# Kernel optimization log

Hardware: AMD Instinct MI355X
Metric: run time of the kernel (lower is better)

The kernel has to match this reference:

```python
import jax, jax.numpy as jnp
import numpy as np

B, S, DIM = 1, 2048, 2048
NH, NKV, HD = 32, 8, 64
NREP = NH // NKV  # 4


def setup_inputs() -> dict:
    key = jax.random.key(0)
    ks = jax.random.split(key, 5)
    x = jax.random.normal(ks[0], (B, S, DIM), jnp.float32)
    # torch nn.Linear weight layout: (out_features, in_features)
    wq = jax.random.normal(ks[1], (NH * HD, DIM), jnp.float32) * (DIM ** -0.5)
    wk = jax.random.normal(ks[2], (NKV * HD, DIM), jnp.float32) * (DIM ** -0.5)
    wv = jax.random.normal(ks[3], (NKV * HD, DIM), jnp.float32) * (DIM ** -0.5)
    wo = jax.random.normal(ks[4], (DIM, NH * HD), jnp.float32) * ((NH * HD) ** -0.5)
    # Llama-style rotary frequencies: angle[t, i] = t / 10000^(2i/head_dim)
    inv_freq = 1.0 / (10000.0 ** (np.arange(0, HD, 2, dtype=np.float64) / HD))  # (HD/2,)
    ang = np.outer(np.arange(S, dtype=np.float64), inv_freq)                     # (S, HD/2)
    freqs_cis = jnp.asarray(np.stack([np.cos(ang), np.sin(ang)], axis=-1), jnp.float32)  # (S, HD/2, 2)
    # additive causal mask, shape (1, 1, S, S)
    mask = jnp.triu(jnp.full((S, S), -1e9, jnp.float32), k=1)[None, None]
    return dict(x=x, wq=wq, wk=wk, wv=wv, wo=wo, freqs_cis=freqs_cis, mask=mask)


def _apply_rope(x, cos, sin):
    # x: (B, S, H, HD); rotate adjacent pairs along last dim
    xr = x.reshape(x.shape[:-1] + (-1, 2))
    x1, x2 = xr[..., 0], xr[..., 1]
    c = cos[None, :, None, :]  # (1, S, 1, HD/2)
    s = sin[None, :, None, :]
    out = jnp.stack([x1 * c - x2 * s, x1 * s + x2 * c], axis=-1)
    return out.reshape(x.shape)


def reference(x, wq, wk, wv, wo, freqs_cis, mask):
    b, s, _ = x.shape
    q = (x @ wq.T).reshape(b, s, NH, HD)
    k = (x @ wk.T).reshape(b, s, NKV, HD)
    v = (x @ wv.T).reshape(b, s, NKV, HD)
    cos, sin = freqs_cis[..., 0], freqs_cis[..., 1]
    q = _apply_rope(q, cos, sin)
    k = _apply_rope(k, cos, sin)
    # GQA: group q heads by kv head instead of materializing repeated K/V
    qg = q.reshape(b, s, NKV, NREP, HD)
    scale = HD ** -0.5
    # scores: (b, g=kv_head, r=rep, s=q_pos, t=k_pos)
    scores = jnp.einsum('bsgrd,btgd->bgrst', qg, k) * scale
    scores = scores + mask[:, :, None]  # (1,1,1,S,S) broadcast
    p = jax.nn.softmax(scores.astype(jnp.float32), axis=-1).astype(q.dtype)
    out = jnp.einsum('bgrst,btgd->bsgrd', p, v).reshape(b, s, NH * HD)
    return out @ wo.T
```

## Files before the change

kernel.cpp:

```cpp
#include <hip/hip_runtime.h>
#include <hip/hip_bf16.h>

#define S_LEN 2048
#define DIM_  2048
#define NH    32
#define NKV   8
#define HD    64

typedef __bf16 bf16x8 __attribute__((ext_vector_type(8)));
typedef __bf16 bf16x4 __attribute__((ext_vector_type(4)));
typedef float  f32x4  __attribute__((ext_vector_type(4)));

#define AS_GLOBAL(p) ((const __attribute__((address_space(1))) void*)(p))
#define AS_LDS(p)    ((__attribute__((address_space(3))) void*)(p))

__global__ __launch_bounds__(256) void cvt_xw(
    const float* __restrict__ x,  const float* __restrict__ wq,
    const float* __restrict__ wk, const float* __restrict__ wv,
    const float* __restrict__ wo,
    __bf16* __restrict__ xb, __bf16* __restrict__ wb, __bf16* __restrict__ wob)
{
  const size_t stride = 458752;
  size_t base = (size_t)blockIdx.x * 256 + threadIdx.x;
#pragma unroll
  for (int k = 0; k < 8; ++k) {
    size_t i = base + (size_t)k * stride;
    const float* src; __bf16* dst; size_t off;
    if (i < 1048576)      { src = x;  dst = xb;            off = i; }
    else if (i < 2097152) { src = wq; dst = wb;            off = i - 1048576; }
    else if (i < 2359296) { src = wk; dst = wb + 4194304;  off = i - 2097152; }
    else if (i < 2621440) { src = wv; dst = wb + 5242880;  off = i - 2359296; }
    else                  { src = wo; dst = wob;           off = i - 2621440; }
    float4 f = ((const float4*)src)[off];
    bf16x4 r;
    r[0] = (__bf16)f.x; r[1] = (__bf16)f.y; r[2] = (__bf16)f.z; r[3] = (__bf16)f.w;
    ((bf16x4*)dst)[off] = r;
  }
}

#define BK 32
#define TA_ELEMS 4096
#define TB_ELEMS 2048

__device__ __forceinline__ void stage_A(
    const __bf16* __restrict__ g, int row0, int k0, int ld, __bf16* lds)
{
  const int tid = threadIdx.x;
  const int wave = tid >> 6;
#pragma unroll
  for (int iss = 0; iss < 2; ++iss) {
    int off = (iss * 256 + tid) * 16;
    int r = off >> 6;
    int c = (off & 63) >> 1;
    __builtin_amdgcn_global_load_lds(
        AS_GLOBAL(g + (size_t)(row0 + r) * ld + k0 + c),
        AS_LDS(lds + iss * 2048 + wave * 512),
        16, 0, 0);
  }
}

__device__ __forceinline__ void stage_B(
    const __bf16* __restrict__ g, int row0, int k0, int ld, __bf16* lds)
{
  const int tid = threadIdx.x;
  int off = tid * 16;
  int r = off >> 6;
  int c = (off & 63) >> 1;
  __builtin_amdgcn_global_load_lds(
      AS_GLOBAL(g + (size_t)(row0 + r) * ld + k0 + c),
      AS_LDS(lds + (tid >> 6) * 512), 16, 0, 0);
}

__device__ __forceinline__ void gemm_mainloop(
    const __bf16* __restrict__ A, const __bf16* __restrict__ B,
    int row0, int col0, int lda, int ldb, int nt,
    __bf16* As, __bf16* Bs, f32x4 acc[4][2])
{
  const int lane = threadIdx.x & 63;
  const int wave = threadIdx.x >> 6;
  const int wr = wave >> 1, wc = wave & 1;
  const int fr = lane & 15, fg = lane >> 4;

  stage_A(A, row0, 0, lda, As);
  stage_B(B, col0, 0, ldb, Bs);

  for (int t = 0; t < nt; ++t) {
    const int cur = t & 1;
    if (t + 1 < nt) {
      stage_A(A, row0, (t + 1) * BK, lda, As + (cur ^ 1) * TA_ELEMS);
      stage_B(B, col0, (t + 1) * BK, ldb, Bs + (cur ^ 1) * TB_ELEMS);
    }
    __syncthreads();
    bf16x8 a[4], b[2];
#pragma unroll
    for (int mi = 0; mi < 4; ++mi)
      a[mi] = *(const bf16x8*)(As + cur * TA_ELEMS + (wr * 64 + mi * 16 + fr) * 32 + fg * 8);
#pragma unroll
    for (int ni = 0; ni < 2; ++ni)
      b[ni] = *(const bf16x8*)(Bs + cur * TB_ELEMS + (wc * 32 + ni * 16 + fr) * 32 + fg * 8);
#pragma unroll
    for (int mi = 0; mi < 4; ++mi)
#pragma unroll
      for (int ni = 0; ni < 2; ++ni)
        acc[mi][ni] = __builtin_amdgcn_mfma_f32_16x16x32_bf16(a[mi], b[ni], acc[mi][ni], 0, 0, 0);
    __syncthreads();
  }
}

__global__ __launch_bounds__(256) void qkv_gemm(
    const __bf16* __restrict__ xb, const __bf16* __restrict__ wb,
    __bf16* __restrict__ q_buf, __bf16* __restrict__ k_buf, __bf16* __restrict__ v_buf)
{
  __shared__ __bf16 As[2 * TA_ELEMS];
  __shared__ __bf16 Bs[2 * TB_ELEMS];
  const int lane = threadIdx.x & 63;
  const int wave = threadIdx.x >> 6;
  const int wr = wave >> 1, wc = wave & 1;
  const int fr = lane & 15, fg = lane >> 4;

  const int lid = blockIdx.x;
  const int xcd = lid & 7;
  const int i   = lid >> 3;
  const int row0 = (i & 15) * 128;
  const int col0 = (xcd * 6 + (i >> 4)) * 64;

  f32x4 acc[4][2] = {};
  gemm_mainloop(xb, wb, row0, col0, DIM_, DIM_, DIM_ / BK, As, Bs, acc);

  const int rowg0 = row0 + wr * 64;
  const int colg0 = col0 + wc * 32;
#pragma unroll
  for (int mi = 0; mi < 4; ++mi) {
#pragma unroll
    for (int ni = 0; ni < 2; ++ni) {
#pragma unroll
      for (int j = 0; j < 4; ++j) {
        int row = rowg0 + mi * 16 + fg * 4 + j;
        int col = colg0 + ni * 16 + fr;
        float v = acc[mi][ni][j];
        if (col < 2048) {
          int h = col >> 6, d = col & 63;
          q_buf[((size_t)h * S_LEN + row) * HD + d] = (__bf16)v;
        } else if (col < 2560) {
          int c = col - 2048, g = c >> 6, d = c & 63;
          k_buf[((size_t)g * S_LEN + row) * HD + d] = (__bf16)v;
        } else {
          int c = col - 2560, g = c >> 6, d = c & 63;
          v_buf[((size_t)g * HD + d) * S_LEN + row] = (__bf16)v;
        }
      }
    }
  }
}

__global__ __launch_bounds__(256) void oproj_gemm(
    const __bf16* __restrict__ attn_buf, const __bf16* __restrict__ wob,
    float* __restrict__ out)
{
  __shared__ __bf16 As[2 * TA_ELEMS];
  __shared__ __bf16 Bs[2 * TB_ELEMS];
  const int lane = threadIdx.x & 63;
  const int wave = threadIdx.x >> 6;
  const int wr = wave >> 1, wc = wave & 1;
  const int fr = lane & 15, fg = lane >> 4;

  const int lid = blockIdx.x;
  const int xcd = lid & 7;
  const int i   = lid >> 3;
  const int row0 = (i & 15) * 128;
  const int col0 = (xcd * 4 + (i >> 4)) * 64;

  f32x4 acc[4][2] = {};
  gemm_mainloop(attn_buf, wob, row0, col0, DIM_, DIM_, DIM_ / BK, As, Bs, acc);

  const int rowg0 = row0 + wr * 64;
  const int colg0 = col0 + wc * 32;
#pragma unroll
  for (int mi = 0; mi < 4; ++mi)
#pragma unroll
    for (int ni = 0; ni < 2; ++ni)
#pragma unroll
      for (int j = 0; j < 4; ++j) {
        int row = rowg0 + mi * 16 + fg * 4 + j;
        int col = colg0 + ni * 16 + fr;
        out[(size_t)row * DIM_ + col] = acc[mi][ni][j];
      }
}

__global__ __launch_bounds__(256) void rope_k(
    __bf16* __restrict__ k_buf, const float* __restrict__ fc)
{
  int idx = blockIdx.x * 256 + threadIdx.x;
  int i    = idx & 31;
  int sp   = (idx >> 5) & (S_LEN - 1);
  int g    = idx >> 16;
  __bf16* buf = k_buf + ((size_t)g * S_LEN + sp) * HD;
  float c = fc[(sp * 32 + i) * 2 + 0];
  float s = fc[(sp * 32 + i) * 2 + 1];
  float x1 = (float)buf[2 * i], x2 = (float)buf[2 * i + 1];
  buf[2 * i + 0] = (__bf16)(x1 * c - x2 * s);
  buf[2 * i + 1] = (__bf16)(x1 * s + x2 * c);
}

__global__ __launch_bounds__(512) void attn_kernel(
    const __bf16* __restrict__ q_buf, const __bf16* __restrict__ k_buf,
    const __bf16* __restrict__ v_buf, const float* __restrict__ fc,
    __bf16* __restrict__ attn_buf)
{
  __shared__ __align__(16) __bf16 Ks[2][64 * 64];
  __shared__ __align__(16) __bf16 Vs[2][64 * 64];
  __shared__ __align__(16) __bf16 lds_p[8][16][72];

  const int tid  = threadIdx.x;
  const int lane = tid & 63;
  const int wave = tid >> 6;
  const int n = blockIdx.x;
  const int qt = (n < 256) ? (15 - (n >> 5)) : ((n - 256) >> 5);
  const int h  = n & 31;
  const int g = h >> 2;
  const int r0 = qt * 128 + wave * 16;
  const int lrow = lane & 15;
  const int lgrp = lane >> 4;
  const int lk = lgrp * 8;

  const __bf16* qh = q_buf + (size_t)h * S_LEN * HD;
  const __bf16* kh = k_buf + (size_t)g * S_LEN * HD;
  const __bf16* vh = v_buf + (size_t)g * HD * S_LEN;

  const int sr   = tid >> 3;
  const int scol = tid & 7;
  const int dcol = scol ^ (sr & 7);

  const float KS = 0.125f * 1.44269504088896f;
  bf16x8 qa[2];
  const float* fcrow = fc + (size_t)(r0 + lrow) * 64;
#pragma unroll
  for (int kk = 0; kk < 2; ++kk) {
    qa[kk] = *(const bf16x8*)(qh + (size_t)(r0 + lrow) * HD + kk * 32 + lk);
    float4 cs0 = *(const float4*)(fcrow + (kk * 16 + lgrp * 4) * 2);
    float4 cs1 = *(const float4*)(fcrow + (kk * 16 + lgrp * 4) * 2 + 4);
    float cc[4] = {cs0.x * KS, cs0.z * KS, cs1.x * KS, cs1.z * KS};
    float ss[4] = {cs0.y * KS, cs0.w * KS, cs1.y * KS, cs1.w * KS};
#pragma unroll
    for (int pr = 0; pr < 4; ++pr) {
      float x1 = (float)qa[kk][2 * pr], x2 = (float)qa[kk][2 * pr + 1];
      qa[kk][2 * pr]     = (__bf16)(x1 * cc[pr] - x2 * ss[pr]);
      qa[kk][2 * pr + 1] = (__bf16)(x1 * ss[pr] + x2 * cc[pr]);
    }
  }

  float m_col = -3.0e38f, l_col = 0.f;
  f32x4 oacc[4] = {};

  const int nt = 2 * qt + 2;

  {
    uint4 k0 = *(const uint4*)(kh + (size_t)sr * HD + scol * 8);
    uint4 v0 = *(const uint4*)(vh + (size_t)sr * S_LEN + scol * 8);
    *(uint4*)(&Ks[0][sr * 64 + dcol * 8]) = k0;
    *(uint4*)(&Vs[0][sr * 64 + dcol * 8]) = v0;
  }
  __syncthreads();

  for (int t = 0; t < nt; ++t) {
    const int cur = t & 1;
    const int t0 = t * 64;

    const int tn0 = (t + 1 < nt ? t + 1 : t) * 64;
    uint4 kreg = *(const uint4*)(kh + (size_t)(tn0 + sr) * HD + scol * 8);
    uint4 vreg = *(const uint4*)(vh + (size_t)sr * S_LEN + tn0 + scol * 8);

    const int dmax = r0 + 15 - t0;
    if (dmax >= 0) {
      f32x4 sc[4] = {};
      const int cmax = dmax >> 4;
      __builtin_amdgcn_s_setprio(1);
#pragma unroll
      for (int c = 0; c < 4; ++c) {
        if (c <= cmax) {
#pragma unroll
          for (int kk = 0; kk < 2; ++kk) {
            bf16x8 ka = *(const bf16x8*)(
                &Ks[cur][(c * 16 + lrow) * 64 + (((kk * 4 + lgrp) ^ (lrow & 7)) * 8)]);
            sc[c] = __builtin_amdgcn_mfma_f32_16x16x32_bf16(ka, qa[kk], sc[c], 0, 0, 0);
          }
        }
      }
      __builtin_amdgcn_s_setprio(0);

      float p[16];
      const int q = r0 + lrow;
      if (t0 + 63 <= r0) {
#pragma unroll
        for (int c = 0; c < 4; ++c)
#pragma unroll
          for (int j = 0; j < 4; ++j)
            p[c * 4 + j] = sc[c][j];
      } else {
#pragma unroll
        for (int c = 0; c < 4; ++c)
#pragma unroll
          for (int j = 0; j < 4; ++j) {
            int kv = t0 + c * 16 + lgrp * 4 + j;
            p[c * 4 + j] = (kv <= q) ? sc[c][j] : -3.0e38f;
          }
      }

      float m8[8];
#pragma unroll
      for (int i = 0; i < 8; ++i) m8[i] = fmaxf(p[i], p[i + 8]);
      float t1 = fmaxf(fmaxf(m8[0], m8[1]), m8[2]);
      float t2 = fmaxf(fmaxf(m8[3], m8[4]), m8[5]);
      float t3 = fmaxf(m8[6], m8[7]);
      float mx = fmaxf(fmaxf(t1, t2), t3);
      mx = fmaxf(mx, __shfl_xor(mx, 16, 64));
      mx = fmaxf(mx, __shfl_xor(mx, 32, 64));

      if (__all(mx <= m_col + 8.f)) {
      } else {
        float nm = fmaxf(m_col, mx);
        float alpha = __builtin_amdgcn_exp2f(m_col - nm);
        m_col = nm;
        float ar[4];
#pragma unroll
        for (int j = 0; j < 4; ++j)
          ar[j] = __shfl(alpha, lgrp * 4 + j, 64);
#pragma unroll
        for (int nf = 0; nf < 4; ++nf)
#pragma unroll
          for (int j = 0; j < 4; ++j)
            oacc[nf][j] *= ar[j];
        l_col *= alpha;
      }

#pragma unroll
      for (int i = 0; i < 16; ++i)
        p[i] = __builtin_amdgcn_exp2f(p[i] - m_col);
      float s8[8], s4[4];
#pragma unroll
      for (int i = 0; i < 8; ++i) s8[i] = p[i] + p[i + 8];
#pragma unroll
      for (int i = 0; i < 4; ++i) s4[i] = s8[i] + s8[i + 4];
      float rs = (s4[0] + s4[1]) + (s4[2] + s4[3]);
      rs += __shfl_xor(rs, 16, 64);
      rs += __shfl_xor(rs, 32, 64);
      l_col += rs;

#pragma unroll
      for (int c = 0; c < 4; ++c)
#pragma unroll
        for (int e = 0; e < 2; ++e) {
          union { __bf16 hh[2]; unsigned u; } pk;
          pk.hh[0] = (__bf16)p[c * 4 + 2 * e];
          pk.hh[1] = (__bf16)p[c * 4 + 2 * e + 1];
          *(unsigned*)&lds_p[wave][lrow][c * 16 + lgrp * 4 + 2 * e] = pk.u;
        }
      asm volatile("s_waitcnt lgkmcnt(0)" ::: "memory");

      bf16x8 pa0 = *(const bf16x8*)&lds_p[wave][lrow][lk];
      __builtin_amdgcn_s_setprio(1);
#pragma unroll
      for (int nf = 0; nf < 4; ++nf) {
        bf16x8 vb = *(const bf16x8*)(
            &Vs[cur][(nf * 16 + lrow) * 64 + ((lgrp ^ (lrow & 7)) * 8)]);
        oacc[nf] = __builtin_amdgcn_mfma_f32_16x16x32_bf16(pa0, vb, oacc[nf], 0, 0, 0);
      }
      __builtin_amdgcn_s_setprio(0);
      if (dmax >= 32) {
        bf16x8 pa1 = *(const bf16x8*)&lds_p[wave][lrow][32 + lk];
        __builtin_amdgcn_s_setprio(1);
#pragma unroll
        for (int nf = 0; nf < 4; ++nf) {
          bf16x8 vb = *(const bf16x8*)(
              &Vs[cur][(nf * 16 + lrow) * 64 + (((4 + lgrp) ^ (lrow & 7)) * 8)]);
          oacc[nf] = __builtin_amdgcn_mfma_f32_16x16x32_bf16(pa1, vb, oacc[nf], 0, 0, 0);
        }
        __builtin_amdgcn_s_setprio(0);
      }
    }

    *(uint4*)(&Ks[cur ^ 1][sr * 64 + dcol * 8]) = kreg;
    *(uint4*)(&Vs[cur ^ 1][sr * 64 + dcol * 8]) = vreg;
    __syncthreads();
  }

  float rlr[4];
#pragma unroll
  for (int j = 0; j < 4; ++j)
    rlr[j] = 1.0f / __shfl(l_col, lgrp * 4 + j, 64);
#pragma unroll
  for (int nf = 0; nf < 4; ++nf)
#pragma unroll
    for (int j = 0; j < 4; ++j) {
      int row = r0 + lgrp * 4 + j;
      attn_buf[(size_t)row * (NH * HD) + h * HD + nf * 16 + lrow] =
          (__bf16)(oacc[nf][j] * rlr[j]);
    }
}

extern "C" void kernel_launch(void* const* d_in, const int* in_sizes, int n_in,
                              void* d_out, int out_size, void* d_ws, size_t ws_size,
                              hipStream_t stream)
{
  const float* x  = (const float*)d_in[0];
  const float* wq = (const float*)d_in[1];
  const float* wk = (const float*)d_in[2];
  const float* wv = (const float*)d_in[3];
  const float* wo = (const float*)d_in[4];
  const float* fc = (const float*)d_in[5];
  float* out = (float*)d_out;

  char* ws = (char*)d_ws;
  __bf16* q_buf    = (__bf16*)(ws);
  __bf16* k_buf    = (__bf16*)(ws +  8u * 1024 * 1024);
  __bf16* v_buf    = (__bf16*)(ws + 10u * 1024 * 1024);
  __bf16* attn_buf = (__bf16*)(ws + 12u * 1024 * 1024);
  __bf16* xb       = (__bf16*)(ws + 20u * 1024 * 1024);
  __bf16* wb       = (__bf16*)(ws + 28u * 1024 * 1024);
  __bf16* wob      = (__bf16*)(ws + 40u * 1024 * 1024);

  cvt_xw<<<dim3(1792), 256, 0, stream>>>(x, wq, wk, wv, wo, xb, wb, wob);
  qkv_gemm<<<dim3(768), 256, 0, stream>>>(xb, wb, q_buf, k_buf, v_buf);
  rope_k<<<dim3(2048), 256, 0, stream>>>(k_buf, fc);
  attn_kernel<<<dim3(512), 512, 0, stream>>>(q_buf, k_buf, v_buf, fc, attn_buf);
  oproj_gemm<<<dim3(512), 256, 0, stream>>>(attn_buf, wob, out);
}
```

Measured before the change: 149.0 us.

## Double GEMM K-tile to 64 and pre-swizzle bf16 operands to avoid LDS bank conflicts

Raises the GEMM K-tile from 32 to 64, which halves the number of main-loop iterations and barriers. The conversion kernel and the attention output store now write bf16 data with an XOR swizzle on 16-byte chunks, so that direct global-to-LDS loads land in a bank-conflict-free layout. The MFMA fragment reads apply the matching XOR. This doubles LDS usage per block, which may reduce occupancy, and it couples the GEMM layout to every producer of its operands.

Result: faster. 136.8 us (-8.2%).

```diff
diff --git a/kernel.cpp b/kernel.cpp
--- a/kernel.cpp
+++ b/kernel.cpp
@@ -14,6 +14,13 @@
 #define AS_GLOBAL(p) ((const __attribute__((address_space(1))) void*)(p))
 #define AS_LDS(p)    ((__attribute__((address_space(3))) void*)(p))
 
+__device__ __forceinline__ bf16x8 pack8(float4 a, float4 b) {
+  bf16x8 r;
+  r[0] = (__bf16)a.x; r[1] = (__bf16)a.y; r[2] = (__bf16)a.z; r[3] = (__bf16)a.w;
+  r[4] = (__bf16)b.x; r[5] = (__bf16)b.y; r[6] = (__bf16)b.z; r[7] = (__bf16)b.w;
+  return r;
+}
+
 __global__ __launch_bounds__(256) void cvt_xw(
     const float* __restrict__ x,  const float* __restrict__ wq,
     const float* __restrict__ wk, const float* __restrict__ wv,
@@ -23,24 +30,23 @@
   const size_t stride = 458752;
   size_t base = (size_t)blockIdx.x * 256 + threadIdx.x;
 #pragma unroll
-  for (int k = 0; k < 8; ++k) {
+  for (int k = 0; k < 4; ++k) {
     size_t i = base + (size_t)k * stride;
-    const float* src; __bf16* dst; size_t off;
-    if (i < 1048576)      { src = x;  dst = xb;            off = i; }
-    else if (i < 2097152) { src = wq; dst = wb;            off = i - 1048576; }
-    else if (i < 2359296) { src = wk; dst = wb + 4194304;  off = i - 2097152; }
-    else if (i < 2621440) { src = wv; dst = wb + 5242880;  off = i - 2359296; }
-    else                  { src = wo; dst = wob;           off = i - 2621440; }
-    float4 f = ((const float4*)src)[off];
-    bf16x4 r;
-    r[0] = (__bf16)f.x; r[1] = (__bf16)f.y; r[2] = (__bf16)f.z; r[3] = (__bf16)f.w;
-    ((bf16x4*)dst)[off] = r;
-  }
-}
-
-#define BK 32
-#define TA_ELEMS 4096
-#define TB_ELEMS 2048
+    const float* src; __bf16* dst; size_t j;
+    if (i < 524288)       { src = x;  dst = xb;            j = i; }
+    else if (i < 1048576) { src = wq; dst = wb;            j = i - 524288; }
+    else if (i < 1179648) { src = wk; dst = wb + 4194304;  j = i - 1048576; }
+    else if (i < 1310720) { src = wv; dst = wb + 5242880;  j = i - 1179648; }
+    else                  { src = wo; dst = wob;           j = i - 1310720; }
+    float4 f0 = ((const float4*)src)[j * 2];
+    float4 f1 = ((const float4*)src)[j * 2 + 1];
+    ((bf16x8*)dst)[j ^ ((j >> 8) & 7)] = pack8(f0, f1);
+  }
+}
+
+#define BK 64
+#define TA_ELEMS 8192
+#define TB_ELEMS 4096
 
 __device__ __forceinline__ void stage_A(
     const __bf16* __restrict__ g, int row0, int k0, int ld, __bf16* lds)
@@ -48,10 +54,10 @@
   const int tid = threadIdx.x;
   const int wave = tid >> 6;
 #pragma unroll
-  for (int iss = 0; iss < 2; ++iss) {
+  for (int iss = 0; iss < 4; ++iss) {
     int off = (iss * 256 + tid) * 16;
-    int r = off >> 6;
-    int c = (off & 63) >> 1;
+    int r = off >> 7;
+    int c = (off & 127) >> 1;
     __builtin_amdgcn_global_load_lds(
         AS_GLOBAL(g + (size_t)(row0 + r) * ld + k0 + c),
         AS_LDS(lds + iss * 2048 + wave * 512),
@@ -63,12 +69,16 @@
     const __bf16* __restrict__ g, int row0, int k0, int ld, __bf16* lds)
 {
   const int tid = threadIdx.x;
-  int off = tid * 16;
-  int r = off >> 6;
-  int c = (off & 63) >> 1;
-  __builtin_amdgcn_global_load_lds(
-      AS_GLOBAL(g + (size_t)(row0 + r) * ld + k0 + c),
-      AS_LDS(lds + (tid >> 6) * 512), 16, 0, 0);
+  const int wave = tid >> 6;
+#pragma unroll
+  for (int iss = 0; iss < 2; ++iss) {
+    int off = (iss * 256 + tid) * 16;
+    int r = off >> 7;
+    int c = (off & 127) >> 1;
+    __builtin_amdgcn_global_load_lds(
+        AS_GLOBAL(g + (size_t)(row0 + r) * ld + k0 + c),
+        AS_LDS(lds + iss * 2048 + wave * 512), 16, 0, 0);
+  }
 }
 
 __device__ __forceinline__ void gemm_mainloop(
@@ -80,6 +90,7 @@
   const int wave = threadIdx.x >> 6;
   const int wr = wave >> 1, wc = wave & 1;
   const int fr = lane & 15, fg = lane >> 4;
+  const int sw = fr & 7;
 
   stage_A(A, row0, 0, lda, As);
   stage_B(B, col0, 0, ldb, Bs);
@@ -91,18 +102,23 @@
       stage_B(B, col0, (t + 1) * BK, ldb, Bs + (cur ^ 1) * TB_ELEMS);
     }
     __syncthreads();
-    bf16x8 a[4], b[2];
-#pragma unroll
-    for (int mi = 0; mi < 4; ++mi)
-      a[mi] = *(const bf16x8*)(As + cur * TA_ELEMS + (wr * 64 + mi * 16 + fr) * 32 + fg * 8);
-#pragma unroll
-    for (int ni = 0; ni < 2; ++ni)
-      b[ni] = *(const bf16x8*)(Bs + cur * TB_ELEMS + (wc * 32 + ni * 16 + fr) * 32 + fg * 8);
-#pragma unroll
-    for (int mi = 0; mi < 4; ++mi)
+#pragma unroll
+    for (int kk = 0; kk < 2; ++kk) {
+      bf16x8 a[4], b[2];
+#pragma unroll
+      for (int mi = 0; mi < 4; ++mi)
+        a[mi] = *(const bf16x8*)(As + cur * TA_ELEMS +
+                 (wr * 64 + mi * 16 + fr) * 64 + (((kk * 4 + fg) ^ sw) * 8));
 #pragma unroll
       for (int ni = 0; ni < 2; ++ni)
-        acc[mi][ni] = __builtin_amdgcn_mfma_f32_16x16x32_bf16(a[mi], b[ni], acc[mi][ni], 0, 0, 0);
+        b[ni] = *(const bf16x8*)(Bs + cur * TB_ELEMS +
+                 (wc * 32 + ni * 16 + fr) * 64 + (((kk * 4 + fg) ^ sw) * 8));
+#pragma unroll
+      for (int mi = 0; mi < 4; ++mi)
+#pragma unroll
+        for (int ni = 0; ni < 2; ++ni)
+          acc[mi][ni] = __builtin_amdgcn_mfma_f32_16x16x32_bf16(a[mi], b[ni], acc[mi][ni], 0, 0, 0);
+    }
     __syncthreads();
   }
 }
@@ -393,7 +409,10 @@
 #pragma unroll
     for (int j = 0; j < 4; ++j) {
       int row = r0 + lgrp * 4 + j;
-      attn_buf[(size_t)row * (NH * HD) + h * HD + nf * 16 + lrow] =
+      int col = h * HD + nf * 16 + lrow;
+      int ch  = (((col >> 3) & 7) ^ (row & 7));
+      int cols = (col & 7) | (ch << 3) | (col & ~63);
+      attn_buf[(size_t)row * (NH * HD) + cols] =
           (__bf16)(oacc[nf][j] * rlr[j]);
     }
 }
```
